# Performance work log

Hardware: AMD Instinct MI355X
Metric: run time of the kernel (lower is better)

Reference implementation:

```python
import jax, jax.numpy as jnp
import numpy as np

B, Dx, Dz, Dy, H = 4096, 512, 512, 256, 2048
T0, T1 = 0.0, 1.0
N_STEPS = 64


def setup_inputs() -> dict:
    key = jax.random.key(0)
    ks = jax.random.split(key, 9)
    X = jax.random.normal(ks[0], (B, Dx), jnp.float32)
    # P sampled Uniform(0.01, 0.1) as in the torch module
    P = jax.random.uniform(ks[1], (Dz, Dx), jnp.float32, 0.01, 0.1)
    # A scaled so spectral radius ~1 -> exp(A*T) stays bounded over the integration
    A = jax.random.normal(ks[2], (Dz, Dz), jnp.float32) * (Dz ** -0.5)
    W1 = jax.random.normal(ks[3], (H, Dz), jnp.float32) * (Dz ** -0.5)
    b1 = jax.random.normal(ks[4], (H,), jnp.float32) * 0.01
    W2 = jax.random.normal(ks[5], (H, H), jnp.float32) * (H ** -0.5)
    b2 = jax.random.normal(ks[6], (H,), jnp.float32) * 0.01
    W3 = jax.random.normal(ks[7], (Dy, H), jnp.float32) * (H ** -0.5)
    b3 = jax.random.normal(ks[8], (Dy,), jnp.float32) * 0.01
    return dict(X=X, P=P, A=A, W1=W1, b1=b1, W2=W2, b2=b2, W3=W3, b3=b3,
                n_steps=N_STEPS)


def reference(X, P, A, W1, b1, W2, b2, W3, b3, n_steps):
    # Z0 = einsum('ji,bi->bj', P, X)  -> projection into latent ODE state
    z0 = X @ P.T  # [B, Dz]
    dt = jnp.float32((T1 - T0) / n_steps)

    def f(z):  # dz/dt = A z, batched: einsum('ji,bi->bj', A, z)
        return z @ A.T

    def rk4_step(z, _):
        k1 = f(z)
        k2 = f(z + 0.5 * dt * k1)
        k3 = f(z + 0.5 * dt * k2)
        k4 = f(z + dt * k3)
        return z + (dt / 6.0) * (k1 + 2.0 * k2 + 2.0 * k3 + k4), None

    zT, _ = jax.lax.scan(rk4_step, z0, None, length=n_steps)  # [B, Dz]

    # QnnMatrixODE MLP head (n_layers=3): Lin+ReLU, Lin+ReLU, Lin
    h = jax.nn.relu(zT @ W1.T + b1)
    h = jax.nn.relu(h @ W2.T + b2)
    y = h @ W3.T + b3  # [B, Dy]
    return y
```

## Files before the change

kernel.cpp:

```cpp
#include <hip/hip_runtime.h>

#define BDIM 4096
#define DX 512
#define DZ 512
#define DY 256
#define HD 2048
#define LDT 72

typedef __attribute__((ext_vector_type(8))) short bf16x8;
typedef __attribute__((ext_vector_type(4))) float f32x4;

__device__ inline unsigned short f2bf(float f) {
    unsigned u = __float_as_uint(f);
    unsigned r = 0x7FFFu + ((u >> 16) & 1u);
    return (unsigned short)((u + r) >> 16);
}
__device__ inline float bf2f(unsigned short h) {
    return __uint_as_float(((unsigned)h) << 16);
}

#define GLDS16(g, l)                                                            \
    __builtin_amdgcn_global_load_lds((const __attribute__((address_space(1))) void*)(g), \
                                     (__attribute__((address_space(3))) void*)(l), 16, 0, 0)

struct PrepJobs {
    const float* src[7];
    unsigned short* hi[7];
    unsigned short* lo[7];
    int n4[7];
};
__global__ __launch_bounds__(256) void prep_k(PrepJobs J) {
    const int j = blockIdx.y;
    if (j < 6) {
        const int i4 = blockIdx.x * 256 + threadIdx.x;
        if (i4 >= J.n4[j]) return;
        float4 v = ((const float4*)J.src[j])[i4];
        ushort4 h;
        h.x = f2bf(v.x); h.y = f2bf(v.y); h.z = f2bf(v.z); h.w = f2bf(v.w);
        ((ushort4*)J.hi[j])[i4] = h;
        if (J.lo[j]) {
            ushort4 l;
            l.x = f2bf(v.x - bf2f(h.x));
            l.y = f2bf(v.y - bf2f(h.y));
            l.z = f2bf(v.z - bf2f(h.z));
            l.w = f2bf(v.w - bf2f(h.w));
            ((ushort4*)J.lo[j])[i4] = l;
        }
    } else {
        if (blockIdx.x >= 256) return;
        __shared__ float t[32][33];
        const float* A = J.src[6];
        unsigned short* HT = J.hi[6];
        unsigned short* LT = J.lo[6];
        const int bx = (blockIdx.x & 15) * 32, by = (blockIdx.x >> 4) * 32;
        const int x = threadIdx.x & 31, y = threadIdx.x >> 5;
#pragma unroll
        for (int dy = 0; dy < 32; dy += 8)
            t[y + dy][x] = A[(size_t)(by + y + dy) * DZ + bx + x];
        __syncthreads();
#pragma unroll
        for (int dy = 0; dy < 32; dy += 8) {
            float v = t[x][y + dy];
            unsigned short h = f2bf(v);
            size_t o = (size_t)(bx + y + dy) * DZ + by + x;
            HT[o] = h;
            LT[o] = f2bf(v - bf2f(h));
        }
    }
}

struct G64In { const unsigned short *Ahi, *Alo, *Bhi, *Blo; const float* Dadd; };
struct G64Out { float* Cf32; unsigned short *Chi, *Clo, *CThi, *CTlo; };
struct E0Out {
    const float* Af32;
    const unsigned short *A2h, *A2l;
    float *B0, *B1, *B2;
    unsigned short *B3h, *B3l;
};

template <int EPI>
__device__ __forceinline__ void g64_core(int bx, int by, int M, int N, int K,
                                         G64In in, G64Out o, E0Out e,
                                         unsigned short* Ash, unsigned short* Asl,
                                         unsigned short* Bsh, unsigned short* Bsl) {
    const int tid = threadIdx.x;
    const int lane = tid & 63;
    const int wave = tid >> 6;
    const int wr = wave >> 1, wc = wave & 1;
    const int row0 = by * 64, col0 = bx * 64;
    const int sr = tid >> 2;
    const int sk = (tid & 3) * 16;

    const int niter = K >> 6;
    bf16x8 pa0, pa1, pl0, pl1, pb0, pb1, pq0, pq1;
    {
        const unsigned short* ar = in.Ahi + (size_t)(row0 + sr) * K + sk;
        const unsigned short* al = in.Alo + (size_t)(row0 + sr) * K + sk;
        const unsigned short* br = in.Bhi + (size_t)(col0 + sr) * K + sk;
        const unsigned short* bl = in.Blo + (size_t)(col0 + sr) * K + sk;
        pa0 = *(const bf16x8*)ar; pa1 = *(const bf16x8*)(ar + 8);
        pl0 = *(const bf16x8*)al; pl1 = *(const bf16x8*)(al + 8);
        pb0 = *(const bf16x8*)br; pb1 = *(const bf16x8*)(br + 8);
        pq0 = *(const bf16x8*)bl; pq1 = *(const bf16x8*)(bl + 8);
    }

    f32x4 acc[4] = {};
    const int mb = wr * 32 + (lane & 15);
    const int nb = wc * 32 + (lane & 15);

    for (int it = 0; it < niter; ++it) {
        __syncthreads();
        *(bf16x8*)&Ash[sr * LDT + sk] = pa0; *(bf16x8*)&Ash[sr * LDT + sk + 8] = pa1;
        *(bf16x8*)&Asl[sr * LDT + sk] = pl0; *(bf16x8*)&Asl[sr * LDT + sk + 8] = pl1;
        *(bf16x8*)&Bsh[sr * LDT + sk] = pb0; *(bf16x8*)&Bsh[sr * LDT + sk + 8] = pb1;
        *(bf16x8*)&Bsl[sr * LDT + sk] = pq0; *(bf16x8*)&Bsl[sr * LDT + sk + 8] = pq1;
        __syncthreads();

        {
            const int kn = (it + 1 < niter) ? ((it + 1) << 6) : 0;
            const unsigned short* ar = in.Ahi + (size_t)(row0 + sr) * K + kn + sk;
            const unsigned short* al = in.Alo + (size_t)(row0 + sr) * K + kn + sk;
            const unsigned short* br = in.Bhi + (size_t)(col0 + sr) * K + kn + sk;
            const unsigned short* bl = in.Blo + (size_t)(col0 + sr) * K + kn + sk;
            pa0 = *(const bf16x8*)ar; pa1 = *(const bf16x8*)(ar + 8);
            pl0 = *(const bf16x8*)al; pl1 = *(const bf16x8*)(al + 8);
            pb0 = *(const bf16x8*)br; pb1 = *(const bf16x8*)(br + 8);
            pq0 = *(const bf16x8*)bl; pq1 = *(const bf16x8*)(bl + 8);
        }

#pragma unroll
        for (int kh = 0; kh < 2; ++kh) {
            const int kk = kh * 32 + (lane >> 4) * 8;
            bf16x8 ah[2], alx[2], bh[2], blx[2];
#pragma unroll
            for (int t = 0; t < 2; ++t) {
                ah[t]  = *(const bf16x8*)&Ash[(mb + t * 16) * LDT + kk];
                alx[t] = *(const bf16x8*)&Asl[(mb + t * 16) * LDT + kk];
                bh[t]  = *(const bf16x8*)&Bsh[(nb + t * 16) * LDT + kk];
                blx[t] = *(const bf16x8*)&Bsl[(nb + t * 16) * LDT + kk];
            }
#pragma unroll
            for (int mt = 0; mt < 2; ++mt)
#pragma unroll
                for (int nt = 0; nt < 2; ++nt) {
                    acc[mt * 2 + nt] = __builtin_amdgcn_mfma_f32_16x16x32_bf16(
                        ah[mt], bh[nt], acc[mt * 2 + nt], 0, 0, 0);
                    acc[mt * 2 + nt] = __builtin_amdgcn_mfma_f32_16x16x32_bf16(
                        ah[mt], blx[nt], acc[mt * 2 + nt], 0, 0, 0);
                    acc[mt * 2 + nt] = __builtin_amdgcn_mfma_f32_16x16x32_bf16(
                        alx[mt], bh[nt], acc[mt * 2 + nt], 0, 0, 0);
                }
        }
    }

#pragma unroll
    for (int mt = 0; mt < 2; ++mt) {
        const int grow = row0 + wr * 32 + mt * 16 + (lane >> 4) * 4;
#pragma unroll
        for (int nt = 0; nt < 2; ++nt) {
            const int gcol = col0 + wc * 32 + nt * 16 + (lane & 15);
            f32x4 a = acc[mt * 2 + nt];
            if (EPI == 1) {
#pragma unroll
                for (int i = 0; i < 4; ++i) {
                    const size_t idx = (size_t)(grow + i) * N + gcol;
                    const float di = (grow + i == gcol) ? 1.0f : 0.0f;
                    const float av = e.Af32[idx];
                    const float a2v = bf2f(e.A2h[idx]) + bf2f(e.A2l[idx]);
                    const float a3v = a[i];
                    e.B0[idx] = di + av + 0.5f * a2v + 1.6666667e-1f * a3v;
                    e.B1[idx] = 4.1666668e-2f * di + 8.3333333e-3f * av +
                                1.3888889e-3f * a2v + 1.9841270e-4f * a3v;
                    e.B2[idx] = 2.4801587e-5f * di + 2.7557319e-6f * av +
                                2.7557319e-7f * a2v + 2.5052108e-8f * a3v;
                    float b3 = 2.0876757e-9f * di + 1.6059044e-10f * av +
                               1.1470746e-11f * a2v + 7.6471637e-13f * a3v;
                    unsigned short hh = f2bf(b3);
                    e.B3h[idx] = hh;
                    e.B3l[idx] = f2bf(b3 - bf2f(hh));
                }
            } else {
                if (in.Dadd) {
#pragma unroll
                    for (int i = 0; i < 4; ++i)
                        a[i] += in.Dadd[(size_t)(grow + i) * N + gcol];
                }
                unsigned short h4[4], l4[4];
#pragma unroll
                for (int i = 0; i < 4; ++i) {
                    h4[i] = f2bf(a[i]);
                    l4[i] = f2bf(a[i] - bf2f(h4[i]));
                }
                if (o.Cf32) {
#pragma unroll
                    for (int i = 0; i < 4; ++i) o.Cf32[(size_t)(grow + i) * N + gcol] = a[i];
                }
                if (o.Chi) {
#pragma unroll
                    for (int i = 0; i < 4; ++i) o.Chi[(size_t)(grow + i) * N + gcol] = h4[i];
                }
                if (o.Clo) {
#pragma unroll
                    for (int i = 0; i < 4; ++i) o.Clo[(size_t)(grow + i) * N + gcol] = l4[i];
                }
                if (o.CThi) {
                    ushort4 u = {h4[0], h4[1], h4[2], h4[3]};
                    *(ushort4*)&o.CThi[(size_t)gcol * M + grow] = u;
                }
                if (o.CTlo) {
                    ushort4 u = {l4[0], l4[1], l4[2], l4[3]};
                    *(ushort4*)&o.CTlo[(size_t)gcol * M + grow] = u;
                }
            }
        }
    }
}

__global__ __launch_bounds__(256) void g64_one(G64In in, G64Out o, int M, int N, int K) {
    __shared__ __align__(16) unsigned short Ash[64 * LDT], Asl[64 * LDT];
    __shared__ __align__(16) unsigned short Bsh[64 * LDT], Bsl[64 * LDT];
    E0Out e = {};
    g64_core<0>(blockIdx.x, blockIdx.y, M, N, K, in, o, e, Ash, Asl, Bsh, Bsl);
}

__global__ __launch_bounds__(256) void g64_dual_e0(G64In i0, E0Out e0o,
                                                   G64In i1, G64Out o1) {
    __shared__ __align__(16) unsigned short Ash[64 * LDT], Asl[64 * LDT];
    __shared__ __align__(16) unsigned short Bsh[64 * LDT], Bsl[64 * LDT];
    if (blockIdx.z == 0) {
        G64Out on = {};
        g64_core<1>(blockIdx.x, blockIdx.y, DZ, DZ, DZ, i0, on, e0o, Ash, Asl, Bsh, Bsl);
    } else {
        E0Out en = {};
        g64_core<0>(blockIdx.x, blockIdx.y, DZ, DZ, DZ, i1, o1, en, Ash, Asl, Bsh, Bsl);
    }
}

template <int RELU, int BIAS, int OUT_BF16>
__global__ __launch_bounds__(256) void gemm_bf16_v2(int M, int N, int K,
                                                    const unsigned short* __restrict__ A,
                                                    const unsigned short* __restrict__ B,
                                                    void* __restrict__ C,
                                                    const float* __restrict__ bias) {
    __shared__ unsigned short As[64 * 32];
    __shared__ unsigned short Bs[128 * 32];

    const int tid = threadIdx.x;
    const int lane = tid & 63;
    const int wave = tid >> 6;
    const int wr = wave >> 1, wc = wave & 1;
    const int row0 = blockIdx.y * 64;
    const int col0 = blockIdx.x * 128;

    const int srow = lane >> 2;
    const int schunk = (lane & 3) * 8;

    f32x4 acc[2][4] = {};

    for (int k0 = 0; k0 < K; k0 += 32) {
        GLDS16(A + (size_t)(row0 + wave * 16 + srow) * K + k0 + schunk, &As[(wave * 16) * 32]);
        GLDS16(B + (size_t)(col0 + wave * 32 + srow) * K + k0 + schunk, &Bs[(wave * 32) * 32]);
        GLDS16(B + (size_t)(col0 + wave * 32 + 16 + srow) * K + k0 + schunk,
               &Bs[(wave * 32 + 16) * 32]);
        __syncthreads();

        const int kk = (lane >> 4) * 8;
        const int mbase = wr * 32 + (lane & 15);
        const int nbase = wc * 64 + (lane & 15);
        bf16x8 af[2], bf[4];
#pragma unroll
        for (int t = 0; t < 2; ++t) af[t] = *(const bf16x8*)&As[(mbase + t * 16) * 32 + kk];
#pragma unroll
        for (int t = 0; t < 4; ++t) bf[t] = *(const bf16x8*)&Bs[(nbase + t * 16) * 32 + kk];
#pragma unroll
        for (int mt = 0; mt < 2; ++mt)
#pragma unroll
            for (int nt = 0; nt < 4; ++nt)
                acc[mt][nt] = __builtin_amdgcn_mfma_f32_16x16x32_bf16(af[mt], bf[nt],
                                                                      acc[mt][nt], 0, 0, 0);
        __syncthreads();
    }

#pragma unroll
    for (int mt = 0; mt < 2; ++mt) {
        const int grow = row0 + wr * 32 + mt * 16 + (lane >> 4) * 4;
#pragma unroll
        for (int nt = 0; nt < 4; ++nt) {
            const int gcol = col0 + wc * 64 + nt * 16 + (lane & 15);
            const float bv = BIAS ? bias[gcol] : 0.0f;
#pragma unroll
            for (int i = 0; i < 4; ++i) {
                float v = acc[mt][nt][i] + bv;
                if (RELU) v = fmaxf(v, 0.0f);
                const size_t off = (size_t)(grow + i) * N + gcol;
                if (OUT_BF16)
                    ((unsigned short*)C)[off] = f2bf(v);
                else
                    ((float*)C)[off] = v;
            }
        }
    }
}

__global__ __launch_bounds__(256) void gemm64nt_y(int M, int N, int K,
                                                  const unsigned short* __restrict__ A,
                                                  const unsigned short* __restrict__ B,
                                                  float* __restrict__ C,
                                                  const float* __restrict__ bias) {
    __shared__ __align__(16) unsigned short As[64 * LDT];
    __shared__ __align__(16) unsigned short Bs[64 * LDT];
    const int tid = threadIdx.x;
    const int lane = tid & 63;
    const int wave = tid >> 6;
    const int wr = wave >> 1, wc = wave & 1;
    const int row0 = blockIdx.y * 64;
    const int col0 = blockIdx.x * 64;
    const int sr = tid >> 2, sk = (tid & 3) * 16;

    const int niter = K >> 6;
    bf16x8 pa0, pa1, pb0, pb1;
    {
        const unsigned short* ar = A + (size_t)(row0 + sr) * K + sk;
        const unsigned short* br = B + (size_t)(col0 + sr) * K + sk;
        pa0 = *(const bf16x8*)ar; pa1 = *(const bf16x8*)(ar + 8);
        pb0 = *(const bf16x8*)br; pb1 = *(const bf16x8*)(br + 8);
    }

    f32x4 acc[4] = {};
    const int mb = wr * 32 + (lane & 15);
    const int nb = wc * 32 + (lane & 15);

    for (int it = 0; it < niter; ++it) {
        __syncthreads();
        *(bf16x8*)&As[sr * LDT + sk] = pa0; *(bf16x8*)&As[sr * LDT + sk + 8] = pa1;
        *(bf16x8*)&Bs[sr * LDT + sk] = pb0; *(bf16x8*)&Bs[sr * LDT + sk + 8] = pb1;
        __syncthreads();

        {
            const int kn = (it + 1 < niter) ? ((it + 1) << 6) : 0;
            const unsigned short* ar = A + (size_t)(row0 + sr) * K + kn + sk;
            const unsigned short* br = B + (size_t)(col0 + sr) * K + kn + sk;
            pa0 = *(const bf16x8*)ar; pa1 = *(const bf16x8*)(ar + 8);
            pb0 = *(const bf16x8*)br; pb1 = *(const bf16x8*)(br + 8);
        }

#pragma unroll
        for (int kh = 0; kh < 2; ++kh) {
            const int kk = kh * 32 + (lane >> 4) * 8;
            bf16x8 af[2], bf[2];
#pragma unroll
            for (int t = 0; t < 2; ++t) {
                af[t] = *(const bf16x8*)&As[(mb + t * 16) * LDT + kk];
                bf[t] = *(const bf16x8*)&Bs[(nb + t * 16) * LDT + kk];
            }
#pragma unroll
            for (int mt = 0; mt < 2; ++mt)
#pragma unroll
                for (int nt = 0; nt < 2; ++nt)
                    acc[mt * 2 + nt] = __builtin_amdgcn_mfma_f32_16x16x32_bf16(
                        af[mt], bf[nt], acc[mt * 2 + nt], 0, 0, 0);
        }
    }

#pragma unroll
    for (int mt = 0; mt < 2; ++mt) {
        const int grow = row0 + wr * 32 + mt * 16 + (lane >> 4) * 4;
#pragma unroll
        for (int nt = 0; nt < 2; ++nt) {
            const int gcol = col0 + wc * 32 + nt * 16 + (lane & 15);
            const float bv = bias ? bias[gcol] : 0.0f;
#pragma unroll
            for (int i = 0; i < 4; ++i)
                C[(size_t)(grow + i) * N + gcol] = acc[mt * 2 + nt][i] + bv;
        }
    }
}

extern "C" void kernel_launch(void* const* d_in, const int* in_sizes, int n_in,
                              void* d_out, int out_size, void* d_ws, size_t ws_size,
                              hipStream_t stream) {
    const float* X  = (const float*)d_in[0];
    const float* P  = (const float*)d_in[1];
    const float* Am = (const float*)d_in[2];
    const float* W1 = (const float*)d_in[3];
    const float* b1 = (const float*)d_in[4];
    const float* W2 = (const float*)d_in[5];
    const float* b2 = (const float*)d_in[6];
    const float* W3 = (const float*)d_in[7];
    const float* b3 = (const float*)d_in[8];
    float* out = (float*)d_out;

    const size_t S = (size_t)DZ * DZ;

    char* p = (char*)d_ws;
    auto alloc_f = [&](size_t n) { float* r = (float*)p; p += n * 4; return r; };
    auto alloc_h = [&](size_t n) { unsigned short* r = (unsigned short*)p; p += ((n * 2 + 15) & ~15ull); return r; };
    unsigned short* Xb   = alloc_h((size_t)BDIM * DX);
    unsigned short* W2b  = alloc_h((size_t)HD * HD);
    unsigned short* W3b  = alloc_h((size_t)DY * HD);
    unsigned short* W1h  = alloc_h((size_t)HD * DZ);
    unsigned short* W1l  = alloc_h((size_t)HD * DZ);
    unsigned short* Pb   = alloc_h(S);
    unsigned short* Ah   = alloc_h(S);
    unsigned short* Al   = alloc_h(S);
    unsigned short* ATh  = alloc_h(S);
    unsigned short* ATl  = alloc_h(S);
    unsigned short* A2h  = alloc_h(S);
    unsigned short* A2l  = alloc_h(S);
    unsigned short* A2Th = alloc_h(S);
    unsigned short* A2Tl = alloc_h(S);
    unsigned short* A4Th = alloc_h(S);
    unsigned short* A4Tl = alloc_h(S);
    float* B0f = alloc_f(S);
    float* B1f = alloc_f(S);
    float* B2f = alloc_f(S);
    unsigned short* B3h  = alloc_h(S);
    unsigned short* B3l  = alloc_h(S);
    unsigned short* H1h  = alloc_h(S);
    unsigned short* H1l  = alloc_h(S);
    unsigned short* H2h  = alloc_h(S);
    unsigned short* H2l  = alloc_h(S);
    unsigned short* H3Th = alloc_h(S);
    unsigned short* H3Tl = alloc_h(S);
    unsigned short* C1b  = alloc_h((size_t)HD * DZ);
    unsigned short* XPb  = alloc_h((size_t)BDIM * DZ);
    unsigned short* h1b  = alloc_h((size_t)BDIM * HD);
    unsigned short* h2b  = alloc_h((size_t)BDIM * HD);

    PrepJobs J;
    J.src[0] = X;  J.hi[0] = Xb;  J.lo[0] = nullptr; J.n4[0] = BDIM * DX / 4;
    J.src[1] = W2; J.hi[1] = W2b; J.lo[1] = nullptr; J.n4[1] = HD * HD / 4;
    J.src[2] = W3; J.hi[2] = W3b; J.lo[2] = nullptr; J.n4[2] = DY * HD / 4;
    J.src[3] = W1; J.hi[3] = W1h; J.lo[3] = W1l;     J.n4[3] = HD * DZ / 4;
    J.src[4] = Am; J.hi[4] = Ah;  J.lo[4] = Al;      J.n4[4] = (int)(S / 4);
    J.src[5] = P;  J.hi[5] = Pb;  J.lo[5] = nullptr; J.n4[5] = (int)(S / 4);
    J.src[6] = Am; J.hi[6] = ATh; J.lo[6] = ATl;     J.n4[6] = 256;
    prep_k<<<dim3(HD * HD / 4 / 256, 7), 256, 0, stream>>>(J);

    gemm_bf16_v2<0, 0, 1><<<dim3(DZ / 128, BDIM / 64), 256, 0, stream>>>(
        BDIM, DZ, DX, Xb, Pb, XPb, nullptr);

    dim3 g8(DZ / 64, DZ / 64);

    {
        G64In i{Ah, Al, ATh, ATl, nullptr};
        G64Out o{nullptr, A2h, A2l, A2Th, A2Tl};
        g64_one<<<g8, 256, 0, stream>>>(i, o, DZ, DZ, DZ);
    }
    {
        G64In i0{A2h, A2l, ATh, ATl, nullptr};
        E0Out e0o{Am, A2h, A2l, B0f, B1f, B2f, B3h, B3l};
        G64In i1{A2h, A2l, A2Th, A2Tl, nullptr};
        G64Out o1{nullptr, nullptr, nullptr, A4Th, A4Tl};
        g64_dual_e0<<<dim3(DZ / 64, DZ / 64, 2), 256, 0, stream>>>(i0, e0o, i1, o1);
    }
    {
        G64In i{B3h, B3l, A4Th, A4Tl, B2f};
        G64Out o{nullptr, H1h, H1l, nullptr, nullptr};
        g64_one<<<g8, 256, 0, stream>>>(i, o, DZ, DZ, DZ);
    }
    {
        G64In i{H1h, H1l, A4Th, A4Tl, B1f};
        G64Out o{nullptr, H2h, H2l, nullptr, nullptr};
        g64_one<<<g8, 256, 0, stream>>>(i, o, DZ, DZ, DZ);
    }
    {
        G64In i{H2h, H2l, A4Th, A4Tl, B0f};
        G64Out o{nullptr, nullptr, nullptr, H3Th, H3Tl};
        g64_one<<<g8, 256, 0, stream>>>(i, o, DZ, DZ, DZ);
    }
    {
        G64In i{W1h, W1l, H3Th, H3Tl, nullptr};
        G64Out o{nullptr, C1b, nullptr, nullptr, nullptr};
        g64_one<<<dim3(DZ / 64, HD / 64), 256, 0, stream>>>(i, o, HD, DZ, DZ);
    }

    gemm_bf16_v2<1, 1, 1><<<dim3(HD / 128, BDIM / 64), 256, 0, stream>>>(
        BDIM, HD, DZ, XPb, C1b, h1b, b1);
    gemm_bf16_v2<1, 1, 1><<<dim3(HD / 128, BDIM / 64), 256, 0, stream>>>(
        BDIM, HD, HD, h1b, W2b, h2b, b2);
    gemm64nt_y<<<dim3(DY / 64, BDIM / 64), 256, 0, stream>>>(
        BDIM, DY, HD, h2b, W3b, out, b3);
}
```

Before: 268.3 us.

## Fold W1 into the matrix-exponential polynomial to shorten the serial GEMM chain

The B0/B1/B2/B3 Horner evaluation of the propagator polynomial in A^4 was a serial chain of 512x512 GEMMs followed by a multiply with W1. The polynomial is now evaluated directly on W1: three independent W1*B_i^T products run in one batched launch, followed by two Horner steps on 2048x512 matrices. This shortens the dependent launch chain and removes the B3 term, trading for extra FLOPs on larger 2048x512 operands and extra workspace. The B coefficient matrices are now stored transposed as hi/lo bf16 pairs.

```diff
diff --git a/kernel.cpp b/kernel.cpp
--- a/kernel.cpp
+++ b/kernel.cpp
@@ -74,8 +74,7 @@
 struct E0Out {
     const float* Af32;
     const unsigned short *A2h, *A2l;
-    float *B0, *B1, *B2;
-    unsigned short *B3h, *B3l;
+    unsigned short *B0Th, *B0Tl, *B1Th, *B1Tl, *B2Th, *B2Tl;
 };
 
 template <int EPI>
@@ -161,6 +160,10 @@
             const int gcol = col0 + wc * 32 + nt * 16 + (lane & 15);
             f32x4 a = acc[mt * 2 + nt];
             if (EPI == 1) {
+                ushort4 h0, l0, h1v, l1v, h2v, l2v;
+                unsigned short* H0 = &h0.x;  unsigned short* L0 = &l0.x;
+                unsigned short* H1 = &h1v.x; unsigned short* L1 = &l1v.x;
+                unsigned short* H2 = &h2v.x; unsigned short* L2 = &l2v.x;
 #pragma unroll
                 for (int i = 0; i < 4; ++i) {
                     const size_t idx = (size_t)(grow + i) * N + gcol;
@@ -168,17 +171,19 @@
                     const float av = e.Af32[idx];
                     const float a2v = bf2f(e.A2h[idx]) + bf2f(e.A2l[idx]);
                     const float a3v = a[i];
-                    e.B0[idx] = di + av + 0.5f * a2v + 1.6666667e-1f * a3v;
-                    e.B1[idx] = 4.1666668e-2f * di + 8.3333333e-3f * av +
-                                1.3888889e-3f * a2v + 1.9841270e-4f * a3v;
-                    e.B2[idx] = 2.4801587e-5f * di + 2.7557319e-6f * av +
-                                2.7557319e-7f * a2v + 2.5052108e-8f * a3v;
-                    float b3 = 2.0876757e-9f * di + 1.6059044e-10f * av +
-                               1.1470746e-11f * a2v + 7.6471637e-13f * a3v;
-                    unsigned short hh = f2bf(b3);
-                    e.B3h[idx] = hh;
-                    e.B3l[idx] = f2bf(b3 - bf2f(hh));
-                }
+                    float b0 = di + av + 0.5f * a2v + 1.6666667e-1f * a3v;
+                    float b1 = 4.1666668e-2f * di + 8.3333333e-3f * av +
+                               1.3888889e-3f * a2v + 1.9841270e-4f * a3v;
+                    float b2 = 2.4801587e-5f * di + 2.7557319e-6f * av +
+                               2.7557319e-7f * a2v + 2.5052108e-8f * a3v;
+                    H0[i] = f2bf(b0); L0[i] = f2bf(b0 - bf2f(H0[i]));
+                    H1[i] = f2bf(b1); L1[i] = f2bf(b1 - bf2f(H1[i]));
+                    H2[i] = f2bf(b2); L2[i] = f2bf(b2 - bf2f(H2[i]));
+                }
+                const size_t to = (size_t)gcol * DZ + grow;
+                *(ushort4*)&e.B0Th[to] = h0; *(ushort4*)&e.B0Tl[to] = l0;
+                *(ushort4*)&e.B1Th[to] = h1v; *(ushort4*)&e.B1Tl[to] = l1v;
+                *(ushort4*)&e.B2Th[to] = h2v; *(ushort4*)&e.B2Tl[to] = l2v;
             } else {
                 if (in.Dadd) {
 #pragma unroll
@@ -234,6 +239,16 @@
         E0Out en = {};
         g64_core<0>(blockIdx.x, blockIdx.y, DZ, DZ, DZ, i1, o1, en, Ash, Asl, Bsh, Bsl);
     }
+}
+
+__global__ __launch_bounds__(256) void g64_tri(G64In i0, G64Out o0, G64In i1, G64Out o1,
+                                               G64In i2, G64Out o2, int M, int N, int K) {
+    __shared__ __align__(16) unsigned short Ash[64 * LDT], Asl[64 * LDT];
+    __shared__ __align__(16) unsigned short Bsh[64 * LDT], Bsl[64 * LDT];
+    E0Out e = {};
+    G64In in = (blockIdx.z == 0) ? i0 : (blockIdx.z == 1) ? i1 : i2;
+    G64Out o = (blockIdx.z == 0) ? o0 : (blockIdx.z == 1) ? o1 : o2;
+    g64_core<0>(blockIdx.x, blockIdx.y, M, N, K, in, o, e, Ash, Asl, Bsh, Bsl);
 }
 
 template <int RELU, int BIAS, int OUT_BF16>
@@ -391,6 +406,7 @@
     float* out = (float*)d_out;
 
     const size_t S = (size_t)DZ * DZ;
+    const size_t SW = (size_t)HD * DZ;
 
     char* p = (char*)d_ws;
     auto alloc_f = [&](size_t n) { float* r = (float*)p; p += n * 4; return r; };
@@ -398,8 +414,8 @@
     unsigned short* Xb   = alloc_h((size_t)BDIM * DX);
     unsigned short* W2b  = alloc_h((size_t)HD * HD);
     unsigned short* W3b  = alloc_h((size_t)DY * HD);
-    unsigned short* W1h  = alloc_h((size_t)HD * DZ);
-    unsigned short* W1l  = alloc_h((size_t)HD * DZ);
+    unsigned short* W1h  = alloc_h(SW);
+    unsigned short* W1l  = alloc_h(SW);
     unsigned short* Pb   = alloc_h(S);
     unsigned short* Ah   = alloc_h(S);
     unsigned short* Al   = alloc_h(S);
@@ -411,18 +427,19 @@
     unsigned short* A2Tl = alloc_h(S);
     unsigned short* A4Th = alloc_h(S);
     unsigned short* A4Tl = alloc_h(S);
-    float* B0f = alloc_f(S);
-    float* B1f = alloc_f(S);
-    float* B2f = alloc_f(S);
-    unsigned short* B3h  = alloc_h(S);
-    unsigned short* B3l  = alloc_h(S);
-    unsigned short* H1h  = alloc_h(S);
-    unsigned short* H1l  = alloc_h(S);
-    unsigned short* H2h  = alloc_h(S);
-    unsigned short* H2l  = alloc_h(S);
-    unsigned short* H3Th = alloc_h(S);
-    unsigned short* H3Tl = alloc_h(S);
-    unsigned short* C1b  = alloc_h((size_t)HD * DZ);
+    unsigned short* B0Th = alloc_h(S);
+    unsigned short* B0Tl = alloc_h(S);
+    unsigned short* B1Th = alloc_h(S);
+    unsigned short* B1Tl = alloc_h(S);
+    unsigned short* B2Th = alloc_h(S);
+    unsigned short* B2Tl = alloc_h(S);
+    float* U0f = alloc_f(SW);
+    float* U1f = alloc_f(SW);
+    unsigned short* U2h  = alloc_h(SW);
+    unsigned short* U2l  = alloc_h(SW);
+    unsigned short* Vh   = alloc_h(SW);
+    unsigned short* Vl   = alloc_h(SW);
+    unsigned short* C1b  = alloc_h(SW);
     unsigned short* XPb  = alloc_h((size_t)BDIM * DZ);
     unsigned short* h1b  = alloc_h((size_t)BDIM * HD);
     unsigned short* h2b  = alloc_h((size_t)BDIM * HD);
@@ -431,7 +448,7 @@
     J.src[0] = X;  J.hi[0] = Xb;  J.lo[0] = nullptr; J.n4[0] = BDIM * DX / 4;
     J.src[1] = W2; J.hi[1] = W2b; J.lo[1] = nullptr; J.n4[1] = HD * HD / 4;
     J.src[2] = W3; J.hi[2] = W3b; J.lo[2] = nullptr; J.n4[2] = DY * HD / 4;
-    J.src[3] = W1; J.hi[3] = W1h; J.lo[3] = W1l;     J.n4[3] = HD * DZ / 4;
+    J.src[3] = W1; J.hi[3] = W1h; J.lo[3] = W1l;     J.n4[3] = (int)(SW / 4);
     J.src[4] = Am; J.hi[4] = Ah;  J.lo[4] = Al;      J.n4[4] = (int)(S / 4);
     J.src[5] = P;  J.hi[5] = Pb;  J.lo[5] = nullptr; J.n4[5] = (int)(S / 4);
     J.src[6] = Am; J.hi[6] = ATh; J.lo[6] = ATl;     J.n4[6] = 256;
@@ -449,28 +466,28 @@
     }
     {
         G64In i0{A2h, A2l, ATh, ATl, nullptr};
-        E0Out e0o{Am, A2h, A2l, B0f, B1f, B2f, B3h, B3l};
+        E0Out e0o{Am, A2h, A2l, B0Th, B0Tl, B1Th, B1Tl, B2Th, B2Tl};
         G64In i1{A2h, A2l, A2Th, A2Tl, nullptr};
         G64Out o1{nullptr, nullptr, nullptr, A4Th, A4Tl};
         g64_dual_e0<<<dim3(DZ / 64, DZ / 64, 2), 256, 0, stream>>>(i0, e0o, i1, o1);
     }
     {
-        G64In i{B3h, B3l, A4Th, A4Tl, B2f};
-        G64Out o{nullptr, H1h, H1l, nullptr, nullptr};
-        g64_one<<<g8, 256, 0, stream>>>(i, o, DZ, DZ, DZ);
-    }
-    {
-        G64In i{H1h, H1l, A4Th, A4Tl, B1f};
-        G64Out o{nullptr, H2h, H2l, nullptr, nullptr};
-        g64_one<<<g8, 256, 0, stream>>>(i, o, DZ, DZ, DZ);
-    }
-    {
-        G64In i{H2h, H2l, A4Th, A4Tl, B0f};
-        G64Out o{nullptr, nullptr, nullptr, H3Th, H3Tl};
-        g64_one<<<g8, 256, 0, stream>>>(i, o, DZ, DZ, DZ);
-    }
-    {
-        G64In i{W1h, W1l, H3Th, H3Tl, nullptr};
+        G64In i0{W1h, W1l, B0Th, B0Tl, nullptr};
+        G64Out o0{U0f, nullptr, nullptr, nullptr, nullptr};
+        G64In i1{W1h, W1l, B1Th, B1Tl, nullptr};
+        G64Out o1{U1f, nullptr, nullptr, nullptr, nullptr};
+        G64In i2{W1h, W1l, B2Th, B2Tl, nullptr};
+        G64Out o2{nullptr, U2h, U2l, nullptr, nullptr};
+        g64_tri<<<dim3(DZ / 64, HD / 64, 3), 256, 0, stream>>>(i0, o0, i1, o1, i2, o2,
+                                                               HD, DZ, DZ);
+    }
+    {
+        G64In i{U2h, U2l, A4Th, A4Tl, U1f};
+        G64Out o{nullptr, Vh, Vl, nullptr, nullptr};
+        g64_one<<<dim3(DZ / 64, HD / 64), 256, 0, stream>>>(i, o, HD, DZ, DZ);
+    }
+    {
+        G64In i{Vh, Vl, A4Th, A4Tl, U0f};
         G64Out o{nullptr, C1b, nullptr, nullptr, nullptr};
         g64_one<<<dim3(DZ / 64, HD / 64), 256, 0, stream>>>(i, o, HD, DZ, DZ);
     }
```

Measured after the change: 263.6 us. No clear change (-1.7%).
